# Kernel tuning notes

Hardware: AMD Instinct MI355X
Metric: run time of the kernel (lower is better)

## Reference

```python
import jax, jax.numpy as jnp
import numpy as np

D = 1024
H = 16
DK = D // H
HID = 4096
EPS = 1e-5


def setup_inputs() -> dict:
    key = jax.random.key(0)
    ks = jax.random.split(key, 16)
    B, S = 2, 2048
    sc = lambda fan_in: 1.0 / np.sqrt(fan_in)
    inp = {
        "x": jax.random.normal(ks[0], (B, S, D), jnp.float32),
        "y": jax.random.normal(ks[1], (B, S, D), jnp.float32),
        "mask": jnp.ones((B, 1, 1, S), jnp.int32),
        # attention projections, stored [in, out]
        "Wq": jax.random.normal(ks[2], (D, D), jnp.float32) * sc(D),
        "bq": jnp.zeros((D,), jnp.float32),
        "Wk": jax.random.normal(ks[3], (D, D), jnp.float32) * sc(D),
        "bk": jnp.zeros((D,), jnp.float32),
        "Wv": jax.random.normal(ks[4], (D, D), jnp.float32) * sc(D),
        "bv": jnp.zeros((D,), jnp.float32),
        "Wo": jax.random.normal(ks[5], (D, D), jnp.float32) * sc(D),
        "bo": jnp.zeros((D,), jnp.float32),
        # FFN
        "W1": jax.random.normal(ks[6], (D, HID), jnp.float32) * sc(D),
        "b1": jnp.zeros((HID,), jnp.float32),
        "W2": jax.random.normal(ks[7], (HID, D), jnp.float32) * sc(HID),
        "b2": jnp.zeros((D,), jnp.float32),
        # LayerNorms
        "g1": jnp.ones((D,), jnp.float32),
        "be1": jnp.zeros((D,), jnp.float32),
        "g2": jnp.ones((D,), jnp.float32),
        "be2": jnp.zeros((D,), jnp.float32),
    }
    return inp


def _layer_norm(x, g, b):
    m = jnp.mean(x, axis=-1, keepdims=True)
    v = jnp.mean(jnp.square(x - m), axis=-1, keepdims=True)
    return (x - m) * jax.lax.rsqrt(v + EPS) * g + b


def _split_heads(t):  # [B,S,D] -> [B,H,S,DK]
    B, S, _ = t.shape
    return t.reshape(B, S, H, DK).transpose(0, 2, 1, 3)


def reference(x, y, mask, Wq, bq, Wk, bk, Wv, bv, Wo, bo,
              W1, b1, W2, b2, g1, be1, g2, be2):
    scale = 1.0 / np.sqrt(DK)
    Q = _split_heads(x @ Wq + bq)
    K = _split_heads(y @ Wk + bk)
    V = _split_heads(y @ Wv + bv)
    scores = jnp.einsum("bhqd,bhkd->bhqk", Q, K) * scale  # [B,H,S,S]
    scores = jnp.where(mask == 0, jnp.float32(-1e9), scores)
    probs = jax.nn.softmax(scores, axis=-1)
    attn = jnp.einsum("bhqk,bhkd->bhqd", probs, V)
    B, _, S, _ = attn.shape
    attn = attn.transpose(0, 2, 1, 3).reshape(B, S, D)
    mha_out = attn @ Wo + bo
    x1 = _layer_norm(x + mha_out, g1, be1)
    ff = jax.nn.relu(x1 @ W1 + b1) @ W2 + b2
    return _layer_norm(x1 + ff, g2, be2)
```

## Files before the change

### kernel.cpp

```cpp
#include <hip/hip_runtime.h>

#define S_ 2048
#define D_ 1024
#define B_ 2
#define H_ 16
#define DK_ 64
#define HID_ 4096

typedef unsigned short u16;
typedef __attribute__((ext_vector_type(8))) short short8;
typedef __attribute__((ext_vector_type(4))) short s16x4;
typedef __attribute__((ext_vector_type(4))) float f32x4;

#define SLOT(q16, r16) (((q16) * 16) + ((r16) ^ (q16)))

__device__ __forceinline__ float bf2f(u16 u) {
  return __uint_as_float(((unsigned int)u) << 16);
}
__device__ __forceinline__ u16 f2bf(float f) {
  unsigned int x = __float_as_uint(f);
  x += 0x7fff + ((x >> 16) & 1);
  return (u16)(x >> 16);
}
__device__ __forceinline__ unsigned int pk2bf(float lo, float hi) {
  return ((__float_as_uint(lo) + 0x8000u) >> 16) | ((__float_as_uint(hi) + 0x8000u) & 0xffff0000u);
}

__device__ __forceinline__ f32x4 mfma16(s16x4 a, s16x4 b, f32x4 c) {
#if __has_builtin(__builtin_amdgcn_mfma_f32_16x16x16_bf16)
  return __builtin_amdgcn_mfma_f32_16x16x16_bf16(a, b, c, 0, 0, 0);
#else
  return __builtin_amdgcn_mfma_f32_16x16x16bf16_1k(a, b, c, 0, 0, 0);
#endif
}

__global__ void prep_k(
    const float* __restrict__ Wq, const float* __restrict__ Wk,
    const float* __restrict__ Wv, const float* __restrict__ Wo,
    const float* __restrict__ W1, const float* __restrict__ W2,
    u16* __restrict__ WqT, u16* __restrict__ WkT, u16* __restrict__ WvT,
    u16* __restrict__ WoT, u16* __restrict__ W1T, u16* __restrict__ W2T) {
  const int z = blockIdx.z;
  __shared__ u16 tile[32][33];
  const float* in; u16* outp; int R, C;
  switch (z) {
    case 0: in = Wq; outp = WqT; R = 1024; C = 1024; break;
    case 1: in = Wk; outp = WkT; R = 1024; C = 1024; break;
    case 2: in = Wv; outp = WvT; R = 1024; C = 1024; break;
    case 3: in = Wo; outp = WoT; R = 1024; C = 1024; break;
    case 4: in = W1; outp = W1T; R = 1024; C = 4096; break;
    default: in = W2; outp = W2T; R = 4096; C = 1024; break;
  }
  int c0, r0;
  if (z == 5) { c0 = blockIdx.y * 32; r0 = blockIdx.x * 32; }
  else        { c0 = blockIdx.x * 32; r0 = blockIdx.y * 32; }
  if (c0 >= C || r0 >= R) return;
  const int tx = threadIdx.x, ty = threadIdx.y;
  for (int i = ty; i < 32; i += 8)
    tile[i][tx] = f2bf(in[(long)(r0 + i) * C + c0 + tx]);
  __syncthreads();
  for (int i = ty; i < 32; i += 8)
    outp[(long)(c0 + i) * R + r0 + tx] = tile[tx][i];
}

__global__ __launch_bounds__(256) void cvt2_k(const float* __restrict__ x, const float* __restrict__ y,
                                              u16* __restrict__ xb, u16* __restrict__ yb) {
  const int z = blockIdx.y;
  const float* in = z ? y : x;
  u16* outp = z ? yb : xb;
  const int i = blockIdx.x * 256 + threadIdx.x;
  float4 v = ((const float4*)in)[i];
  unsigned int lo = (unsigned int)f2bf(v.x) | ((unsigned int)f2bf(v.y) << 16);
  unsigned int hi = (unsigned int)f2bf(v.z) | ((unsigned int)f2bf(v.w) << 16);
  ((uint2*)outp)[i] = make_uint2(lo, hi);
}

template<int MT, int NT, int OUTF32>
__global__ __launch_bounds__(256) void gemm_bt(
    const u16* __restrict__ A, const u16* __restrict__ Bt,
    const float* __restrict__ bias, void* __restrict__ Cv,
    int K, int lda, int ldb, int ldc,
    long sA, long sB, long sC, int relu) {
  constexpr int BM = MT * 32;
  constexpr int BN = NT * 32;
  __shared__ __align__(16) u16 As[BM * 32];
  __shared__ __align__(16) u16 Bs[BN * 32];
  const int z = blockIdx.z;
  A  += (long)z * sA;
  Bt += (long)z * sB;
  const int tid  = threadIdx.x;
  const int lane = tid & 63, wave = tid >> 6;
  const int quad = lane >> 4, l15 = lane & 15;
  const int wm = wave >> 1, wn = wave & 1;
  const u16* Ab = A  + (long)(blockIdx.y * BM) * lda;
  const u16* Bb = Bt + (long)(blockIdx.x * BN) * ldb;

  f32x4 acc[MT][NT];
#pragma unroll
  for (int i = 0; i < MT; ++i)
#pragma unroll
    for (int j = 0; j < NT; ++j) acc[i][j] = (f32x4){0.f, 0.f, 0.f, 0.f};

  const int r0  = tid >> 2;
  const int kk0 = (tid & 3) * 8;

  for (int kt = 0; kt < K; kt += 32) {
#pragma unroll
    for (int p = 0; p < BM / 64; ++p) {
      __builtin_amdgcn_global_load_lds(
          (const __attribute__((address_space(1))) void*)(Ab + (long)(p * 64 + r0) * lda + kt + kk0),
          (__attribute__((address_space(3))) void*)(&As[p * 2048 + tid * 8]), 16, 0, 0);
    }
#pragma unroll
    for (int p = 0; p < BN / 64; ++p) {
      __builtin_amdgcn_global_load_lds(
          (const __attribute__((address_space(1))) void*)(Bb + (long)(p * 64 + r0) * ldb + kt + kk0),
          (__attribute__((address_space(3))) void*)(&Bs[p * 2048 + tid * 8]), 16, 0, 0);
    }
    __syncthreads();
    short8 af[MT], bfr[NT];
#pragma unroll
    for (int mt = 0; mt < MT; ++mt)
      af[mt] = *(const short8*)&As[(wm * (MT * 16) + mt * 16 + l15) * 32 + quad * 8];
#pragma unroll
    for (int nt = 0; nt < NT; ++nt)
      bfr[nt] = *(const short8*)&Bs[(wn * (NT * 16) + nt * 16 + l15) * 32 + quad * 8];
#pragma unroll
    for (int mt = 0; mt < MT; ++mt)
#pragma unroll
      for (int nt = 0; nt < NT; ++nt)
        acc[mt][nt] = __builtin_amdgcn_mfma_f32_16x16x32_bf16(af[mt], bfr[nt], acc[mt][nt], 0, 0, 0);
    __syncthreads();
  }

#pragma unroll
  for (int nt = 0; nt < NT; ++nt) {
    const int col = blockIdx.x * BN + wn * (NT * 16) + nt * 16 + l15;
    const float bvv = bias ? bias[col] : 0.f;
#pragma unroll
    for (int mt = 0; mt < MT; ++mt) {
#pragma unroll
      for (int r = 0; r < 4; ++r) {
        const int row = blockIdx.y * BM + wm * (MT * 16) + mt * 16 + quad * 4 + r;
        float v = acc[mt][nt][r] + bvv;
        if (relu) v = fmaxf(v, 0.f);
        if (OUTF32) ((float*)Cv)[(long)z * sC + (long)row * ldc + col] = v;
        else        ((u16*)Cv)[(long)z * sC + (long)row * ldc + col] = f2bf(v);
      }
    }
  }
}

template<int RELU, int MODE>
__global__ __launch_bounds__(512, 2) void gemm256_k(
    const u16* __restrict__ A, const u16* __restrict__ Bt,
    const float* __restrict__ bias, u16* __restrict__ C,
    int K, int lda, int ldb, int ldc, int kOff, long sC) {
  __shared__ __align__(16) u16 lds[65536];
  int bx, by, z;
  if (MODE == 1) {
    const int gid = blockIdx.y * 16 + blockIdx.x;
    const int xcd = gid & 7, idx = gid >> 3;
    by = (xcd & 3) * 4 + (idx & 3);
    bx = (xcd >> 2) * 8 + (idx >> 2);
    z = 0;
  } else if (MODE == 2) {
    const int gid = (blockIdx.z * 16 + blockIdx.y) * 4 + blockIdx.x;
    const int xcd = gid & 7, idx = gid >> 3;
    z = idx >> 3;
    const int sub = idx & 7;
    by = xcd * 2 + (sub & 1);
    bx = sub >> 1;
  } else {
    bx = blockIdx.x; by = blockIdx.y; z = blockIdx.z;
  }
  A  += (long)z * kOff;
  Bt += (long)z * kOff;
  const int tid = threadIdx.x;
  const int lane = tid & 63, w = tid >> 6;
  const int quad = lane >> 4, l15 = lane & 15;
  const int wm = w >> 2, wn = w & 3;

  const int srow = w * 16 + l15;
  const u16* a0p = A + (long)(by * 256 + srow) * lda + quad * 8;
  const u16* a1p = a0p + (long)128 * lda;
  const u16* b0p = Bt + (long)(bx * 256 + srow) * ldb + quad * 8;
  const u16* b1p = b0p + (long)128 * ldb;

  f32x4 acc[8][4];
#pragma unroll
  for (int i = 0; i < 8; ++i)
#pragma unroll
    for (int j = 0; j < 4; ++j) acc[i][j] = (f32x4){0.f, 0.f, 0.f, 0.f};

  auto STAGE = [&](int c) {
    const int sl = (c & 3) * 8192;
    const long ko = (long)c * 32;
    __builtin_amdgcn_global_load_lds(
        (const __attribute__((address_space(1))) void*)(a0p + ko),
        (__attribute__((address_space(3))) void*)(&lds[sl + tid * 8]), 16, 0, 0);
    __builtin_amdgcn_global_load_lds(
        (const __attribute__((address_space(1))) void*)(a1p + ko),
        (__attribute__((address_space(3))) void*)(&lds[sl + 4096 + tid * 8]), 16, 0, 0);
    __builtin_amdgcn_global_load_lds(
        (const __attribute__((address_space(1))) void*)(b0p + ko),
        (__attribute__((address_space(3))) void*)(&lds[32768 + sl + tid * 8]), 16, 0, 0);
    __builtin_amdgcn_global_load_lds(
        (const __attribute__((address_space(1))) void*)(b1p + ko),
        (__attribute__((address_space(3))) void*)(&lds[32768 + sl + 4096 + tid * 8]), 16, 0, 0);
  };

  auto COMPUTE = [&](int t) {
    const int sl = (t & 3) * 8192;
    short8 af[8], bfv[4];
#pragma unroll
    for (int fr = 0; fr < 8; ++fr)
      af[fr] = *(const short8*)&lds[sl + ((wm * 8 + fr) * 64 + lane) * 8];
#pragma unroll
    for (int fc = 0; fc < 4; ++fc)
      bfv[fc] = *(const short8*)&lds[32768 + sl + ((wn * 4 + fc) * 64 + lane) * 8];
    __builtin_amdgcn_s_setprio(1);
#pragma unroll
    for (int fr = 0; fr < 8; ++fr)
#pragma unroll
      for (int fc = 0; fc < 4; ++fc)
        acc[fr][fc] = __builtin_amdgcn_mfma_f32_16x16x32_bf16(af[fr], bfv[fc], acc[fr][fc], 0, 0, 0);
    __builtin_amdgcn_s_setprio(0);
  };

  const int NT = K >> 5;
  STAGE(0); STAGE(1); STAGE(2);
  for (int t = 0; t < NT - 2; ++t) {
    asm volatile("s_waitcnt vmcnt(8)" ::: "memory");
    __builtin_amdgcn_s_barrier();
    __builtin_amdgcn_sched_barrier(0);
    if (t + 3 < NT) STAGE(t + 3);
    COMPUTE(t);
  }
  asm volatile("s_waitcnt vmcnt(4)" ::: "memory");
  __builtin_amdgcn_s_barrier();
  __builtin_amdgcn_sched_barrier(0);
  COMPUTE(NT - 2);
  asm volatile("s_waitcnt vmcnt(0)" ::: "memory");
  __builtin_amdgcn_s_barrier();
  __builtin_amdgcn_sched_barrier(0);
  COMPUTE(NT - 1);

  C += (long)z * sC;
#pragma unroll
  for (int fc = 0; fc < 4; ++fc) {
    const int col = bx * 256 + wn * 64 + fc * 16 + l15;
    const float bvv = bias ? bias[col] : 0.f;
#pragma unroll
    for (int fr = 0; fr < 8; ++fr) {
      const long row = by * 256 + wm * 128 + fr * 16 + quad * 4;
#pragma unroll
      for (int r = 0; r < 4; ++r) {
        float v = acc[fr][fc][r] + bvv;
        if (RELU) v = fmaxf(v, 0.f);
        C[(row + r) * ldc + col] = f2bf(v);
      }
    }
  }
}

__global__ __launch_bounds__(256) void qkv_k(
    const u16* __restrict__ xb, const u16* __restrict__ yb,
    const u16* __restrict__ WqT, const u16* __restrict__ WkT, const u16* __restrict__ WvT,
    const float* __restrict__ bq, const float* __restrict__ bk, const float* __restrict__ bv,
    u16* __restrict__ Q, u16* __restrict__ Kp, u16* __restrict__ Vp) {
  __shared__ __align__(16) u16 As[128 * 32];
  __shared__ __align__(16) u16 Bs[128 * 32];
  const int z = blockIdx.z;
  const u16* A  = (z == 0) ? xb : yb;
  const u16* Bt = (z == 0) ? WqT : (z == 1) ? WkT : WvT;
  const float* bias = (z == 0) ? bq : (z == 1) ? bk : bv;
  u16* C = (z == 0) ? Q : (z == 1) ? Kp : Vp;
  const float sc = (z == 0) ? 0.18033688011112042f : 1.0f;
  const int tid  = threadIdx.x;
  const int lane = tid & 63, wave = tid >> 6;
  const int quad = lane >> 4, l15 = lane & 15;
  const int wm = wave >> 1, wn = wave & 1;
  const u16* Ab = A  + (long)(blockIdx.y * 128) * D_;
  const u16* Bb = Bt + (long)(blockIdx.x * 128) * D_;

  f32x4 acc[4][4];
#pragma unroll
  for (int i = 0; i < 4; ++i)
#pragma unroll
    for (int j = 0; j < 4; ++j) acc[i][j] = (f32x4){0.f, 0.f, 0.f, 0.f};

  const int r0  = tid >> 2;
  const int kk0 = (tid & 3) * 8;

  for (int kt = 0; kt < D_; kt += 32) {
#pragma unroll
    for (int p = 0; p < 2; ++p) {
      __builtin_amdgcn_global_load_lds(
          (const __attribute__((address_space(1))) void*)(Ab + (long)(p * 64 + r0) * D_ + kt + kk0),
          (__attribute__((address_space(3))) void*)(&As[p * 2048 + tid * 8]), 16, 0, 0);
      __builtin_amdgcn_global_load_lds(
          (const __attribute__((address_space(1))) void*)(Bb + (long)(p * 64 + r0) * D_ + kt + kk0),
          (__attribute__((address_space(3))) void*)(&Bs[p * 2048 + tid * 8]), 16, 0, 0);
    }
    __syncthreads();
    short8 af[4], bfr[4];
#pragma unroll
    for (int mt = 0; mt < 4; ++mt)
      af[mt] = *(const short8*)&As[(wm * 64 + mt * 16 + l15) * 32 + quad * 8];
#pragma unroll
    for (int nt = 0; nt < 4; ++nt)
      bfr[nt] = *(const short8*)&Bs[(wn * 64 + nt * 16 + l15) * 32 + quad * 8];
#pragma unroll
    for (int mt = 0; mt < 4; ++mt)
#pragma unroll
      for (int nt = 0; nt < 4; ++nt)
        acc[mt][nt] = __builtin_amdgcn_mfma_f32_16x16x32_bf16(af[mt], bfr[nt], acc[mt][nt], 0, 0, 0);
    __syncthreads();
  }

#pragma unroll
  for (int nt = 0; nt < 4; ++nt) {
    const int col = blockIdx.x * 128 + wn * 64 + nt * 16 + l15;
    const float bvv = bias[col];
#pragma unroll
    for (int mt = 0; mt < 4; ++mt) {
#pragma unroll
      for (int r = 0; r < 4; ++r) {
        const int row = blockIdx.y * 128 + wm * 64 + mt * 16 + quad * 4 + r;
        C[(long)row * D_ + col] = f2bf((acc[mt][nt][r] + bvv) * sc);
      }
    }
  }
}

__global__ void vtrans_k(const u16* __restrict__ V, u16* __restrict__ Vt) {
  __shared__ u16 tile[32][33];
  const int bh = blockIdx.z, b = bh >> 4, h = bh & 15;
  const u16* in = V + (long)b * S_ * D_ + h * DK_;
  u16* outp = Vt + (long)bh * DK_ * S_;
  const int s0 = blockIdx.x * 32, d0 = blockIdx.y * 32;
  const int tx = threadIdx.x, ty = threadIdx.y;
  for (int i = ty; i < 32; i += 8)
    tile[i][tx] = in[(long)(s0 + i) * D_ + d0 + tx];
  __syncthreads();
  for (int i = ty; i < 32; i += 8)
    outp[(long)(d0 + i) * S_ + s0 + tx] = tile[tx][i];
}

__global__ __launch_bounds__(256, 4) void flash_k(
    const u16* __restrict__ Q, const u16* __restrict__ Kp, const u16* __restrict__ Vt,
    const int* __restrict__ mask, u16* __restrict__ ctx) {
  __shared__ __align__(16) u16 sQ[8192];
  __shared__ __align__(16) u16 sK[2][2048];
  __shared__ __align__(16) u16 sV[2][2048];
  __shared__ int s_allones;

  const int bh = blockIdx.x, qt = blockIdx.y;
  const int b = bh >> 4, h = bh & 15;
  const int tid = threadIdx.x;
  const int w = tid >> 6, lane = tid & 63;
  const int quad = lane >> 4, l15 = lane & 15;

  const u16* Qg  = Q  + ((long)b * S_ + qt * 128) * D_ + h * DK_;
  const u16* Kg  = Kp + (long)b * S_ * D_ + h * DK_;
  const u16* Vtg = Vt + (long)bh * DK_ * S_;
  const int* maskg = mask + (long)b * S_;
  u16* ctxg = ctx + ((long)b * S_ + qt * 128) * D_ + h * DK_;

  const int krow = tid >> 3, kc = tid & 7;
  const u16* kptr = Kg + (long)krow * D_ + kc * 8;
  const int ksw = (((krow >> 4) * 2 + (kc >> 2)) * 64 + SLOT(kc & 3, krow & 15)) * 8;
  const int vd  = ((tid >> 6) << 4) | (tid & 15);
  const int vq4 = ((tid >> 4) & 3) * 4;
  const u16* vptr = Vtg + (long)vd * S_ + vq4;

  uint4 kreg = *(const uint4*)kptr;
  uint2 vlo = *(const uint2*)vptr;
  uint2 vhi = *(const uint2*)(vptr + 16);

  int part = 1;
  for (int i = tid; i < S_; i += 256) part &= (maskg[i] != 0);
  if (tid == 0) s_allones = 1;

#pragma unroll
  for (int p = 0; p < 4; ++p) {
    const int idx = p * 256 + tid;
    const int row = idx >> 3, cb = idx & 7;
    uint4 v = *(const uint4*)(Qg + (long)row * D_ + cb * 8);
    *(uint4*)&sQ[(((row >> 4) * 2 + (cb >> 2)) * 64 + SLOT(cb & 3, row & 15)) * 8] = v;
  }
  *(uint4*)&sK[0][ksw] = kreg;
  *(uint4*)&sV[0][tid * 8] = make_uint4(vlo.x, vlo.y, vhi.x, vhi.y);
  kreg = *(const uint4*)(kptr + 32 * D_);
  vlo = *(const uint2*)(vptr + 32);
  vhi = *(const uint2*)(vptr + 48);
  kptr += 64 * D_;
  vptr += 64;
  __syncthreads();

  const int rslot = SLOT(quad, l15) * 8;

  short8 qf[2][2];
#pragma unroll
  for (int mf = 0; mf < 2; ++mf)
#pragma unroll
    for (int kt = 0; kt < 2; ++kt)
      qf[mf][kt] = *(const short8*)&sQ[(((w * 2 + mf) * 2 + kt) * 64) * 8 + rslot];

  if (!part) s_allones = 0;
  __syncthreads();
  const int allones = s_allones;

  float lsum[2] = {0.f, 0.f};
  f32x4 accOT[2][4];
#pragma unroll
  for (int i = 0; i < 2; ++i)
#pragma unroll
    for (int j = 0; j < 4; ++j) accOT[i][j] = (f32x4){0.f, 0.f, 0.f, 0.f};

  for (int t = 0; t < 64; ++t) {
    if (t) __syncthreads();
    const int buf = t & 1, nb = buf ^ 1;
    if (t < 63) {
      *(uint4*)&sK[nb][ksw] = kreg;
      *(uint4*)&sV[nb][tid * 8] = make_uint4(vlo.x, vlo.y, vhi.x, vhi.y);
      if (t < 62) {
        kreg = *(const uint4*)kptr;
        vlo = *(const uint2*)vptr;
        vhi = *(const uint2*)(vptr + 16);
        kptr += 32 * D_;
        vptr += 32;
      }
    }
    f32x4 accS[2][2];
#pragma unroll
    for (int i = 0; i < 2; ++i)
#pragma unroll
      for (int j = 0; j < 2; ++j) accS[i][j] = (f32x4){0.f, 0.f, 0.f, 0.f};
#pragma unroll
    for (int kt = 0; kt < 2; ++kt) {
      short8 kf0 = *(const short8*)&sK[buf][(kt * 64) * 8 + rslot];
      short8 kf1 = *(const short8*)&sK[buf][((2 + kt) * 64) * 8 + rslot];
#pragma unroll
      for (int mf = 0; mf < 2; ++mf) {
        accS[0][mf] = __builtin_amdgcn_mfma_f32_16x16x32_bf16(kf0, qf[mf][kt], accS[0][mf], 0, 0, 0);
        accS[1][mf] = __builtin_amdgcn_mfma_f32_16x16x32_bf16(kf1, qf[mf][kt], accS[1][mf], 0, 0, 0);
      }
    }
    s16x4 pb[2][2];
    if (allones) {
#pragma unroll
      for (int mk = 0; mk < 2; ++mk)
#pragma unroll
        for (int mf = 0; mf < 2; ++mf) {
          float p0 = __builtin_amdgcn_exp2f(accS[mk][mf][0]);
          float p1 = __builtin_amdgcn_exp2f(accS[mk][mf][1]);
          float p2 = __builtin_amdgcn_exp2f(accS[mk][mf][2]);
          float p3 = __builtin_amdgcn_exp2f(accS[mk][mf][3]);
          lsum[mf] += (p0 + p1) + (p2 + p3);
          *(uint2*)&pb[mk][mf] = make_uint2(pk2bf(p0, p1), pk2bf(p2, p3));
        }
    } else {
      const int4 mv0 = *(const int4*)(maskg + t * 32 + quad * 4);
      const int4 mv1 = *(const int4*)(maskg + t * 32 + 16 + quad * 4);
#pragma unroll
      for (int mk = 0; mk < 2; ++mk) {
        const int4 mv = mk ? mv1 : mv0;
#pragma unroll
        for (int mf = 0; mf < 2; ++mf) {
          float p0 = mv.x ? __builtin_amdgcn_exp2f(accS[mk][mf][0]) : 0.f;
          float p1 = mv.y ? __builtin_amdgcn_exp2f(accS[mk][mf][1]) : 0.f;
          float p2 = mv.z ? __builtin_amdgcn_exp2f(accS[mk][mf][2]) : 0.f;
          float p3 = mv.w ? __builtin_amdgcn_exp2f(accS[mk][mf][3]) : 0.f;
          lsum[mf] += (p0 + p1) + (p2 + p3);
          *(uint2*)&pb[mk][mf] = make_uint2(pk2bf(p0, p1), pk2bf(p2, p3));
        }
      }
    }
#pragma unroll
    for (int n = 0; n < 4; ++n) {
      short8 vv = *(const short8*)&sV[buf][(n * 64 + lane) * 8];
      s16x4 v0 = __builtin_shufflevector(vv, vv, 0, 1, 2, 3);
      s16x4 v1 = __builtin_shufflevector(vv, vv, 4, 5, 6, 7);
#pragma unroll
      for (int mf = 0; mf < 2; ++mf) {
        accOT[mf][n] = mfma16(v0, pb[0][mf], accOT[mf][n]);
        accOT[mf][n] = mfma16(v1, pb[1][mf], accOT[mf][n]);
      }
    }
  }

#pragma unroll
  for (int mf = 0; mf < 2; ++mf) {
    lsum[mf] += __shfl_xor(lsum[mf], 16, 64);
    lsum[mf] += __shfl_xor(lsum[mf], 32, 64);
  }
  const float inv0 = 1.f / lsum[0], inv1 = 1.f / lsum[1];
#pragma unroll
  for (int mf = 0; mf < 2; ++mf) {
    const float iv = mf ? inv1 : inv0;
    u16* cp = ctxg + (long)(w * 32 + mf * 16 + l15) * D_;
#pragma unroll
    for (int n = 0; n < 4; ++n) {
      float o0 = accOT[mf][n][0] * iv;
      float o1 = accOT[mf][n][1] * iv;
      float o2 = accOT[mf][n][2] * iv;
      float o3 = accOT[mf][n][3] * iv;
      *(uint2*)(cp + n * 16 + quad * 4) = make_uint2(pk2bf(o0, o1), pk2bf(o2, o3));
    }
  }
}

__device__ __forceinline__ float block_reduce_sum(float v, float* red) {
#pragma unroll
  for (int off = 32; off; off >>= 1) v += __shfl_down(v, off, 64);
  __syncthreads();
  if ((threadIdx.x & 63) == 0) red[threadIdx.x >> 6] = v;
  __syncthreads();
  return red[0] + red[1] + red[2] + red[3];
}

__global__ __launch_bounds__(256) void addln_fb(const float* __restrict__ A,
    const u16* __restrict__ M0, const u16* __restrict__ M1, const float* __restrict__ bo,
    const float* __restrict__ g, const float* __restrict__ be, u16* __restrict__ outp) {
  __shared__ float red[4];
  const int row = blockIdx.x, tid = threadIdx.x;
  const float4 av = ((const float4*)(A + (long)row * D_))[tid];
  const uint2 m0 = ((const uint2*)(M0 + (long)row * D_))[tid];
  const uint2 m1 = ((const uint2*)(M1 + (long)row * D_))[tid];
  const int c0 = tid * 4;
  float xv[4];
  xv[0] = av.x + bf2f((u16)(m0.x & 0xffff)) + bf2f((u16)(m1.x & 0xffff)) + bo[c0 + 0];
  xv[1] = av.y + bf2f((u16)(m0.x >> 16))    + bf2f((u16)(m1.x >> 16))    + bo[c0 + 1];
  xv[2] = av.z + bf2f((u16)(m0.y & 0xffff)) + bf2f((u16)(m1.y & 0xffff)) + bo[c0 + 2];
  xv[3] = av.w + bf2f((u16)(m0.y >> 16))    + bf2f((u16)(m1.y >> 16))    + bo[c0 + 3];
  float s  = xv[0] + xv[1] + xv[2] + xv[3];
  float ss = xv[0]*xv[0] + xv[1]*xv[1] + xv[2]*xv[2] + xv[3]*xv[3];
  s  = block_reduce_sum(s, red);
  ss = block_reduce_sum(ss, red);
  const float m   = s * (1.0f / 1024.0f);
  const float var = ss * (1.0f / 1024.0f) - m * m;
  const float rs  = rsqrtf(var + 1e-5f);
  float v0 = (xv[0] - m) * rs * g[c0 + 0] + be[c0 + 0];
  float v1 = (xv[1] - m) * rs * g[c0 + 1] + be[c0 + 1];
  float v2 = (xv[2] - m) * rs * g[c0 + 2] + be[c0 + 2];
  float v3 = (xv[3] - m) * rs * g[c0 + 3] + be[c0 + 3];
  unsigned int o01 = (unsigned int)f2bf(v0) | ((unsigned int)f2bf(v1) << 16);
  unsigned int o23 = (unsigned int)f2bf(v2) | ((unsigned int)f2bf(v3) << 16);
  ((uint2*)(outp + (long)row * D_))[tid] = make_uint2(o01, o23);
}

__global__ __launch_bounds__(256) void addln2_bf(const u16* __restrict__ A,
    const u16* __restrict__ F0, const u16* __restrict__ F1,
    const u16* __restrict__ F2, const u16* __restrict__ F3,
    const float* __restrict__ b2,
    const float* __restrict__ g, const float* __restrict__ be, float* __restrict__ outp) {
  __shared__ float red[4];
  const int row = blockIdx.x, tid = threadIdx.x;
  const uint2 av = ((const uint2*)(A + (long)row * D_))[tid];
  const uint2 f0 = ((const uint2*)(F0 + (long)row * D_))[tid];
  const uint2 f1 = ((const uint2*)(F1 + (long)row * D_))[tid];
  const uint2 f2 = ((const uint2*)(F2 + (long)row * D_))[tid];
  const uint2 f3 = ((const uint2*)(F3 + (long)row * D_))[tid];
  const int c0 = tid * 4;
  float xv[4];
  xv[0] = bf2f((u16)(av.x & 0xffff)) + bf2f((u16)(f0.x & 0xffff)) + bf2f((u16)(f1.x & 0xffff))
        + bf2f((u16)(f2.x & 0xffff)) + bf2f((u16)(f3.x & 0xffff)) + b2[c0 + 0];
  xv[1] = bf2f((u16)(av.x >> 16))    + bf2f((u16)(f0.x >> 16))    + bf2f((u16)(f1.x >> 16))
        + bf2f((u16)(f2.x >> 16))    + bf2f((u16)(f3.x >> 16))    + b2[c0 + 1];
  xv[2] = bf2f((u16)(av.y & 0xffff)) + bf2f((u16)(f0.y & 0xffff)) + bf2f((u16)(f1.y & 0xffff))
        + bf2f((u16)(f2.y & 0xffff)) + bf2f((u16)(f3.y & 0xffff)) + b2[c0 + 2];
  xv[3] = bf2f((u16)(av.y >> 16))    + bf2f((u16)(f0.y >> 16))    + bf2f((u16)(f1.y >> 16))
        + bf2f((u16)(f2.y >> 16))    + bf2f((u16)(f3.y >> 16))    + b2[c0 + 3];
  float s  = xv[0] + xv[1] + xv[2] + xv[3];
  float ss = xv[0]*xv[0] + xv[1]*xv[1] + xv[2]*xv[2] + xv[3]*xv[3];
  s  = block_reduce_sum(s, red);
  ss = block_reduce_sum(ss, red);
  const float m   = s * (1.0f / 1024.0f);
  const float var = ss * (1.0f / 1024.0f) - m * m;
  const float rs  = rsqrtf(var + 1e-5f);
  float4 o;
  o.x = (xv[0] - m) * rs * g[c0 + 0] + be[c0 + 0];
  o.y = (xv[1] - m) * rs * g[c0 + 1] + be[c0 + 1];
  o.z = (xv[2] - m) * rs * g[c0 + 2] + be[c0 + 2];
  o.w = (xv[3] - m) * rs * g[c0 + 3] + be[c0 + 3];
  ((float4*)(outp + (long)row * D_))[tid] = o;
}

extern "C" void kernel_launch(void* const* d_in, const int* in_sizes, int n_in,
                              void* d_out, int out_size, void* d_ws, size_t ws_size,
                              hipStream_t stream) {
  const float* x   = (const float*)d_in[0];
  const float* y   = (const float*)d_in[1];
  const int* mask  = (const int*)d_in[2];
  const float* Wq = (const float*)d_in[3];  const float* bq = (const float*)d_in[4];
  const float* Wk = (const float*)d_in[5];  const float* bk = (const float*)d_in[6];
  const float* Wv = (const float*)d_in[7];  const float* bv = (const float*)d_in[8];
  const float* Wo = (const float*)d_in[9];  const float* bo = (const float*)d_in[10];
  const float* W1 = (const float*)d_in[11]; const float* b1 = (const float*)d_in[12];
  const float* W2 = (const float*)d_in[13]; const float* b2 = (const float*)d_in[14];
  const float* g1 = (const float*)d_in[15]; const float* be1 = (const float*)d_in[16];
  const float* g2 = (const float*)d_in[17]; const float* be2 = (const float*)d_in[18];
  float* out = (float*)d_out;

  char* w = (char*)d_ws;
  const size_t MB = 1024 * 1024;
  u16* WqT = (u16*)(w + 0 * MB);
  u16* WkT = (u16*)(w + 2 * MB);
  u16* WvT = (u16*)(w + 4 * MB);
  u16* WoT = (u16*)(w + 6 * MB);
  u16* W1T = (u16*)(w + 8 * MB);
  u16* W2T = (u16*)(w + 16 * MB);
  u16* xb  = (u16*)(w + 24 * MB);
  u16* yb  = (u16*)(w + 32 * MB);
  u16* Q   = (u16*)(w + 40 * MB);
  u16* Kp  = (u16*)(w + 48 * MB);
  u16* Vp  = (u16*)(w + 56 * MB);
  u16* Vt  = (u16*)(w + 64 * MB);
  u16* ctx = (u16*)(w + 72 * MB);
  u16* mha = (u16*)(w + 80 * MB);
  u16* x1  = (u16*)(w + 24 * MB);
  u16* h1  = (u16*)(w + 96 * MB);
  u16* ff  = (u16*)(w + 40 * MB);

  prep_k<<<dim3(128, 32, 6), dim3(32, 8), 0, stream>>>(Wq, Wk, Wv, Wo, W1, W2,
      WqT, WkT, WvT, WoT, W1T, W2T);
  cvt2_k<<<dim3(4096, 2), 256, 0, stream>>>(x, y, xb, yb);

  qkv_k<<<dim3(8, 32, 3), 256, 0, stream>>>(xb, yb, WqT, WkT, WvT, bq, bk, bv, Q, Kp, Vp);

  vtrans_k<<<dim3(64, 2, 32), dim3(32, 8), 0, stream>>>(Vp, Vt);

  flash_k<<<dim3(32, 16), 256, 0, stream>>>(Q, Kp, Vt, mask, ctx);

  gemm_bt<4, 4, 0><<<dim3(8, 32, 2), 256, 0, stream>>>(ctx, WoT, nullptr, mha,
      512, 1024, 1024, 1024, 512, 512, (long)4096 * 1024, 0);
  addln_fb<<<dim3(4096), 256, 0, stream>>>(x, mha, mha + (long)4096 * 1024, bo, g1, be1, x1);

  gemm256_k<1, 1><<<dim3(16, 16, 1), 512, 0, stream>>>(x1, W1T, b1, h1,
      1024, 1024, 1024, 4096, 0, 0);
  gemm256_k<0, 2><<<dim3(4, 16, 4), 512, 0, stream>>>(h1, W2T, nullptr, ff,
      1024, 4096, 4096, 1024, 1024, (long)4096 * 1024);
  addln2_bf<<<dim3(4096), 256, 0, stream>>>(x1, ff, ff + (long)4096 * 1024,
      ff + (long)2 * 4096 * 1024, ff + (long)3 * 4096 * 1024, b2, g2, be2, out);
}
```

Measured before the change: 397.0 us.

## Halve flash attention query tile and drop XCD-aware GEMM block remapping

The flash attention kernel now handles 64 query rows per block instead of 128, so each wave covers 16 rows and the grid doubles to 1024 blocks. This cuts registers and shared memory per block and may allow higher occupancy. In exchange, K/V tiles are loaded twice as often per query row. Separately, the FFN GEMMs drop their XCD-aware block-index swizzle and use plain blockIdx mapping, which gives up L2 locality across chiplets.

```diff
diff --git a/kernel.cpp b/kernel.cpp
--- a/kernel.cpp
+++ b/kernel.cpp
@@ -151,29 +151,13 @@
   }
 }
 
-template<int RELU, int MODE>
+template<int RELU>
 __global__ __launch_bounds__(512, 2) void gemm256_k(
     const u16* __restrict__ A, const u16* __restrict__ Bt,
     const float* __restrict__ bias, u16* __restrict__ C,
     int K, int lda, int ldb, int ldc, int kOff, long sC) {
   __shared__ __align__(16) u16 lds[65536];
-  int bx, by, z;
-  if (MODE == 1) {
-    const int gid = blockIdx.y * 16 + blockIdx.x;
-    const int xcd = gid & 7, idx = gid >> 3;
-    by = (xcd & 3) * 4 + (idx & 3);
-    bx = (xcd >> 2) * 8 + (idx >> 2);
-    z = 0;
-  } else if (MODE == 2) {
-    const int gid = (blockIdx.z * 16 + blockIdx.y) * 4 + blockIdx.x;
-    const int xcd = gid & 7, idx = gid >> 3;
-    z = idx >> 3;
-    const int sub = idx & 7;
-    by = xcd * 2 + (sub & 1);
-    bx = sub >> 1;
-  } else {
-    bx = blockIdx.x; by = blockIdx.y; z = blockIdx.z;
-  }
+  const int bx = blockIdx.x, by = blockIdx.y, z = blockIdx.z;
   A  += (long)z * kOff;
   Bt += (long)z * kOff;
   const int tid = threadIdx.x;
@@ -351,7 +335,7 @@
 __global__ __launch_bounds__(256, 4) void flash_k(
     const u16* __restrict__ Q, const u16* __restrict__ Kp, const u16* __restrict__ Vt,
     const int* __restrict__ mask, u16* __restrict__ ctx) {
-  __shared__ __align__(16) u16 sQ[8192];
+  __shared__ __align__(16) u16 sQ[4096];
   __shared__ __align__(16) u16 sK[2][2048];
   __shared__ __align__(16) u16 sV[2][2048];
   __shared__ int s_allones;
@@ -362,11 +346,11 @@
   const int w = tid >> 6, lane = tid & 63;
   const int quad = lane >> 4, l15 = lane & 15;
 
-  const u16* Qg  = Q  + ((long)b * S_ + qt * 128) * D_ + h * DK_;
+  const u16* Qg  = Q  + ((long)b * S_ + qt * 64) * D_ + h * DK_;
   const u16* Kg  = Kp + (long)b * S_ * D_ + h * DK_;
   const u16* Vtg = Vt + (long)bh * DK_ * S_;
   const int* maskg = mask + (long)b * S_;
-  u16* ctxg = ctx + ((long)b * S_ + qt * 128) * D_ + h * DK_;
+  u16* ctxg = ctx + ((long)b * S_ + qt * 64) * D_ + h * DK_;
 
   const int krow = tid >> 3, kc = tid & 7;
   const u16* kptr = Kg + (long)krow * D_ + kc * 8;
@@ -384,7 +368,7 @@
   if (tid == 0) s_allones = 1;
 
 #pragma unroll
-  for (int p = 0; p < 4; ++p) {
+  for (int p = 0; p < 2; ++p) {
     const int idx = p * 256 + tid;
     const int row = idx >> 3, cb = idx & 7;
     uint4 v = *(const uint4*)(Qg + (long)row * D_ + cb * 8);
@@ -401,23 +385,19 @@
 
   const int rslot = SLOT(quad, l15) * 8;
 
-  short8 qf[2][2];
-#pragma unroll
-  for (int mf = 0; mf < 2; ++mf)
-#pragma unroll
-    for (int kt = 0; kt < 2; ++kt)
-      qf[mf][kt] = *(const short8*)&sQ[(((w * 2 + mf) * 2 + kt) * 64) * 8 + rslot];
+  short8 qf[2];
+#pragma unroll
+  for (int kt = 0; kt < 2; ++kt)
+    qf[kt] = *(const short8*)&sQ[((w * 2 + kt) * 64) * 8 + rslot];
 
   if (!part) s_allones = 0;
   __syncthreads();
   const int allones = s_allones;
 
-  float lsum[2] = {0.f, 0.f};
-  f32x4 accOT[2][4];
-#pragma unroll
-  for (int i = 0; i < 2; ++i)
-#pragma unroll
-    for (int j = 0; j < 4; ++j) accOT[i][j] = (f32x4){0.f, 0.f, 0.f, 0.f};
+  float lsum = 0.f;
+  f32x4 accOT[4];
+#pragma unroll
+  for (int j = 0; j < 4; ++j) accOT[j] = (f32x4){0.f, 0.f, 0.f, 0.f};
 
   for (int t = 0; t < 64; ++t) {
     if (t) __syncthreads();
@@ -433,49 +413,39 @@
         vptr += 32;
       }
     }
-    f32x4 accS[2][2];
-#pragma unroll
-    for (int i = 0; i < 2; ++i)
-#pragma unroll
-      for (int j = 0; j < 2; ++j) accS[i][j] = (f32x4){0.f, 0.f, 0.f, 0.f};
+    f32x4 accS[2];
+    accS[0] = (f32x4){0.f, 0.f, 0.f, 0.f};
+    accS[1] = (f32x4){0.f, 0.f, 0.f, 0.f};
 #pragma unroll
     for (int kt = 0; kt < 2; ++kt) {
       short8 kf0 = *(const short8*)&sK[buf][(kt * 64) * 8 + rslot];
       short8 kf1 = *(const short8*)&sK[buf][((2 + kt) * 64) * 8 + rslot];
-#pragma unroll
-      for (int mf = 0; mf < 2; ++mf) {
-        accS[0][mf] = __builtin_amdgcn_mfma_f32_16x16x32_bf16(kf0, qf[mf][kt], accS[0][mf], 0, 0, 0);
-        accS[1][mf] = __builtin_amdgcn_mfma_f32_16x16x32_bf16(kf1, qf[mf][kt], accS[1][mf], 0, 0, 0);
+      accS[0] = __builtin_amdgcn_mfma_f32_16x16x32_bf16(kf0, qf[kt], accS[0], 0, 0, 0);
+      accS[1] = __builtin_amdgcn_mfma_f32_16x16x32_bf16(kf1, qf[kt], accS[1], 0, 0, 0);
+    }
+    s16x4 pb[2];
+    if (allones) {
+#pragma unroll
+      for (int mk = 0; mk < 2; ++mk) {
+        float p0 = __builtin_amdgcn_exp2f(accS[mk][0]);
+        float p1 = __builtin_amdgcn_exp2f(accS[mk][1]);
+        float p2 = __builtin_amdgcn_exp2f(accS[mk][2]);
+        float p3 = __builtin_amdgcn_exp2f(accS[mk][3]);
+        lsum += (p0 + p1) + (p2 + p3);
+        *(uint2*)&pb[mk] = make_uint2(pk2bf(p0, p1), pk2bf(p2, p3));
       }
-    }
-    s16x4 pb[2][2];
-    if (allones) {
-#pragma unroll
-      for (int mk = 0; mk < 2; ++mk)
-#pragma unroll
-        for (int mf = 0; mf < 2; ++mf) {
-          float p0 = __builtin_amdgcn_exp2f(accS[mk][mf][0]);
-          float p1 = __builtin_amdgcn_exp2f(accS[mk][mf][1]);
-          float p2 = __builtin_amdgcn_exp2f(accS[mk][mf][2]);
-          float p3 = __builtin_amdgcn_exp2f(accS[mk][mf][3]);
-          lsum[mf] += (p0 + p1) + (p2 + p3);
-          *(uint2*)&pb[mk][mf] = make_uint2(pk2bf(p0, p1), pk2bf(p2, p3));
-        }
     } else {
       const int4 mv0 = *(const int4*)(maskg + t * 32 + quad * 4);
       const int4 mv1 = *(const int4*)(maskg + t * 32 + 16 + quad * 4);
 #pragma unroll
       for (int mk = 0; mk < 2; ++mk) {
         const int4 mv = mk ? mv1 : mv0;
-#pragma unroll
-        for (int mf = 0; mf < 2; ++mf) {
-          float p0 = mv.x ? __builtin_amdgcn_exp2f(accS[mk][mf][0]) : 0.f;
-          float p1 = mv.y ? __builtin_amdgcn_exp2f(accS[mk][mf][1]) : 0.f;
-          float p2 = mv.z ? __builtin_amdgcn_exp2f(accS[mk][mf][2]) : 0.f;
-          float p3 = mv.w ? __builtin_amdgcn_exp2f(accS[mk][mf][3]) : 0.f;
-          lsum[mf] += (p0 + p1) + (p2 + p3);
-          *(uint2*)&pb[mk][mf] = make_uint2(pk2bf(p0, p1), pk2bf(p2, p3));
-        }
+        float p0 = mv.x ? __builtin_amdgcn_exp2f(accS[mk][0]) : 0.f;
+        float p1 = mv.y ? __builtin_amdgcn_exp2f(accS[mk][1]) : 0.f;
+        float p2 = mv.z ? __builtin_amdgcn_exp2f(accS[mk][2]) : 0.f;
+        float p3 = mv.w ? __builtin_amdgcn_exp2f(accS[mk][3]) : 0.f;
+        lsum += (p0 + p1) + (p2 + p3);
+        *(uint2*)&pb[mk] = make_uint2(pk2bf(p0, p1), pk2bf(p2, p3));
       }
     }
 #pragma unroll
@@ -483,32 +453,22 @@
       short8 vv = *(const short8*)&sV[buf][(n * 64 + lane) * 8];
       s16x4 v0 = __builtin_shufflevector(vv, vv, 0, 1, 2, 3);
       s16x4 v1 = __builtin_shufflevector(vv, vv, 4, 5, 6, 7);
-#pragma unroll
-      for (int mf = 0; mf < 2; ++mf) {
-        accOT[mf][n] = mfma16(v0, pb[0][mf], accOT[mf][n]);
-        accOT[mf][n] = mfma16(v1, pb[1][mf], accOT[mf][n]);
-      }
-    }
-  }
-
-#pragma unroll
-  for (int mf = 0; mf < 2; ++mf) {
-    lsum[mf] += __shfl_xor(lsum[mf], 16, 64);
-    lsum[mf] += __shfl_xor(lsum[mf], 32, 64);
-  }
-  const float inv0 = 1.f / lsum[0], inv1 = 1.f / lsum[1];
-#pragma unroll
-  for (int mf = 0; mf < 2; ++mf) {
-    const float iv = mf ? inv1 : inv0;
-    u16* cp = ctxg + (long)(w * 32 + mf * 16 + l15) * D_;
-#pragma unroll
-    for (int n = 0; n < 4; ++n) {
-      float o0 = accOT[mf][n][0] * iv;
-      float o1 = accOT[mf][n][1] * iv;
-      float o2 = accOT[mf][n][2] * iv;
-      float o3 = accOT[mf][n][3] * iv;
-      *(uint2*)(cp + n * 16 + quad * 4) = make_uint2(pk2bf(o0, o1), pk2bf(o2, o3));
-    }
+      accOT[n] = mfma16(v0, pb[0], accOT[n]);
+      accOT[n] = mfma16(v1, pb[1], accOT[n]);
+    }
+  }
+
+  lsum += __shfl_xor(lsum, 16, 64);
+  lsum += __shfl_xor(lsum, 32, 64);
+  const float iv = 1.f / lsum;
+  u16* cp = ctxg + (long)(w * 16 + l15) * D_;
+#pragma unroll
+  for (int n = 0; n < 4; ++n) {
+    float o0 = accOT[n][0] * iv;
+    float o1 = accOT[n][1] * iv;
+    float o2 = accOT[n][2] * iv;
+    float o3 = accOT[n][3] * iv;
+    *(uint2*)(cp + n * 16 + quad * 4) = make_uint2(pk2bf(o0, o1), pk2bf(o2, o3));
   }
 }
 
@@ -632,15 +592,15 @@
 
   vtrans_k<<<dim3(64, 2, 32), dim3(32, 8), 0, stream>>>(Vp, Vt);
 
-  flash_k<<<dim3(32, 16), 256, 0, stream>>>(Q, Kp, Vt, mask, ctx);
+  flash_k<<<dim3(32, 32), 256, 0, stream>>>(Q, Kp, Vt, mask, ctx);
 
   gemm_bt<4, 4, 0><<<dim3(8, 32, 2), 256, 0, stream>>>(ctx, WoT, nullptr, mha,
       512, 1024, 1024, 1024, 512, 512, (long)4096 * 1024, 0);
   addln_fb<<<dim3(4096), 256, 0, stream>>>(x, mha, mha + (long)4096 * 1024, bo, g1, be1, x1);
 
-  gemm256_k<1, 1><<<dim3(16, 16, 1), 512, 0, stream>>>(x1, W1T, b1, h1,
+  gemm256_k<1><<<dim3(16, 16, 1), 512, 0, stream>>>(x1, W1T, b1, h1,
       1024, 1024, 1024, 4096, 0, 0);
-  gemm256_k<0, 2><<<dim3(4, 16, 4), 512, 0, stream>>>(h1, W2T, nullptr, ff,
+  gemm256_k<0><<<dim3(4, 16, 4), 512, 0, stream>>>(h1, W2T, nullptr, ff,
       1024, 4096, 4096, 1024, 1024, (long)4096 * 1024);
   addln2_bf<<<dim3(4096), 256, 0, stream>>>(x1, ff, ff + (long)4096 * 1024,
       ff + (long)2 * 4096 * 1024, ff + (long)3 * 4096 * 1024, b2, g2, be2, out);
```

New measurement: 415.5 us. +4.7%, slower.

## Widen flash blocks to 512 threads, split K/V loading, fuse prep kernels

Applied to the files above, without the earlier changes.

The flash attention kernel now runs 512-thread blocks that each cover 256 query rows. The first half of the threads stages K tiles and the second half stages V tiles, so each thread issues a single load per iteration, and the grid is halved. The activation bf16 conversion is folded into the weight-transpose kernel to save one launch. The XCD-aware block remapping in the FFN GEMMs is removed in favour of plain block indices, which may hurt L2 locality across chiplets. Fewer, larger flash blocks also lower occupancy flexibility and CU coverage.

```diff
diff --git a/kernel.cpp b/kernel.cpp
--- a/kernel.cpp
+++ b/kernel.cpp
@@ -34,14 +34,28 @@
 #endif
 }
 
-__global__ void prep_k(
+__global__ void prep8_k(
     const float* __restrict__ Wq, const float* __restrict__ Wk,
     const float* __restrict__ Wv, const float* __restrict__ Wo,
     const float* __restrict__ W1, const float* __restrict__ W2,
+    const float* __restrict__ x, const float* __restrict__ y,
     u16* __restrict__ WqT, u16* __restrict__ WkT, u16* __restrict__ WvT,
-    u16* __restrict__ WoT, u16* __restrict__ W1T, u16* __restrict__ W2T) {
+    u16* __restrict__ WoT, u16* __restrict__ W1T, u16* __restrict__ W2T,
+    u16* __restrict__ xb, u16* __restrict__ yb) {
+  __shared__ u16 tile[32][33];
   const int z = blockIdx.z;
-  __shared__ u16 tile[32][33];
+  const int tx = threadIdx.x, ty = threadIdx.y;
+  if (z >= 6) {
+    const float* in = (z == 7) ? y : x;
+    u16* outp = (z == 7) ? yb : xb;
+    const int tid = ty * 32 + tx;
+    const long i = ((long)blockIdx.y * 128 + blockIdx.x) * 256 + tid;
+    float4 v = ((const float4*)in)[i];
+    unsigned int lo = (unsigned int)f2bf(v.x) | ((unsigned int)f2bf(v.y) << 16);
+    unsigned int hi = (unsigned int)f2bf(v.z) | ((unsigned int)f2bf(v.w) << 16);
+    ((uint2*)outp)[i] = make_uint2(lo, hi);
+    return;
+  }
   const float* in; u16* outp; int R, C;
   switch (z) {
     case 0: in = Wq; outp = WqT; R = 1024; C = 1024; break;
@@ -55,24 +69,11 @@
   if (z == 5) { c0 = blockIdx.y * 32; r0 = blockIdx.x * 32; }
   else        { c0 = blockIdx.x * 32; r0 = blockIdx.y * 32; }
   if (c0 >= C || r0 >= R) return;
-  const int tx = threadIdx.x, ty = threadIdx.y;
   for (int i = ty; i < 32; i += 8)
     tile[i][tx] = f2bf(in[(long)(r0 + i) * C + c0 + tx]);
   __syncthreads();
   for (int i = ty; i < 32; i += 8)
     outp[(long)(c0 + i) * R + r0 + tx] = tile[tx][i];
-}
-
-__global__ __launch_bounds__(256) void cvt2_k(const float* __restrict__ x, const float* __restrict__ y,
-                                              u16* __restrict__ xb, u16* __restrict__ yb) {
-  const int z = blockIdx.y;
-  const float* in = z ? y : x;
-  u16* outp = z ? yb : xb;
-  const int i = blockIdx.x * 256 + threadIdx.x;
-  float4 v = ((const float4*)in)[i];
-  unsigned int lo = (unsigned int)f2bf(v.x) | ((unsigned int)f2bf(v.y) << 16);
-  unsigned int hi = (unsigned int)f2bf(v.z) | ((unsigned int)f2bf(v.w) << 16);
-  ((uint2*)outp)[i] = make_uint2(lo, hi);
 }
 
 template<int MT, int NT, int OUTF32>
@@ -151,29 +152,13 @@
   }
 }
 
-template<int RELU, int MODE>
+template<int RELU>
 __global__ __launch_bounds__(512, 2) void gemm256_k(
     const u16* __restrict__ A, const u16* __restrict__ Bt,
     const float* __restrict__ bias, u16* __restrict__ C,
     int K, int lda, int ldb, int ldc, int kOff, long sC) {
   __shared__ __align__(16) u16 lds[65536];
-  int bx, by, z;
-  if (MODE == 1) {
-    const int gid = blockIdx.y * 16 + blockIdx.x;
-    const int xcd = gid & 7, idx = gid >> 3;
-    by = (xcd & 3) * 4 + (idx & 3);
-    bx = (xcd >> 2) * 8 + (idx >> 2);
-    z = 0;
-  } else if (MODE == 2) {
-    const int gid = (blockIdx.z * 16 + blockIdx.y) * 4 + blockIdx.x;
-    const int xcd = gid & 7, idx = gid >> 3;
-    z = idx >> 3;
-    const int sub = idx & 7;
-    by = xcd * 2 + (sub & 1);
-    bx = sub >> 1;
-  } else {
-    bx = blockIdx.x; by = blockIdx.y; z = blockIdx.z;
-  }
+  const int bx = blockIdx.x, by = blockIdx.y, z = blockIdx.z;
   A  += (long)z * kOff;
   Bt += (long)z * kOff;
   const int tid = threadIdx.x;
@@ -348,10 +333,10 @@
     outp[(long)(d0 + i) * S_ + s0 + tx] = tile[tx][i];
 }
 
-__global__ __launch_bounds__(256, 4) void flash_k(
+__global__ __launch_bounds__(512, 2) void flash_k(
     const u16* __restrict__ Q, const u16* __restrict__ Kp, const u16* __restrict__ Vt,
     const int* __restrict__ mask, u16* __restrict__ ctx) {
-  __shared__ __align__(16) u16 sQ[8192];
+  __shared__ __align__(16) u16 sQ[16384];
   __shared__ __align__(16) u16 sK[2][2048];
   __shared__ __align__(16) u16 sV[2][2048];
   __shared__ int s_allones;
@@ -362,41 +347,52 @@
   const int w = tid >> 6, lane = tid & 63;
   const int quad = lane >> 4, l15 = lane & 15;
 
-  const u16* Qg  = Q  + ((long)b * S_ + qt * 128) * D_ + h * DK_;
+  const u16* Qg  = Q  + ((long)b * S_ + qt * 256) * D_ + h * DK_;
   const u16* Kg  = Kp + (long)b * S_ * D_ + h * DK_;
   const u16* Vtg = Vt + (long)bh * DK_ * S_;
   const int* maskg = mask + (long)b * S_;
-  u16* ctxg = ctx + ((long)b * S_ + qt * 128) * D_ + h * DK_;
-
-  const int krow = tid >> 3, kc = tid & 7;
-  const u16* kptr = Kg + (long)krow * D_ + kc * 8;
+  u16* ctxg = ctx + ((long)b * S_ + qt * 256) * D_ + h * DK_;
+
+  const int isK = tid < 256;
+  const int t2 = tid & 255;
+  const int krow = t2 >> 3, kc = t2 & 7;
+  const int vd  = ((t2 >> 6) << 4) | (t2 & 15);
+  const int vq4 = ((t2 >> 4) & 3) * 4;
+  const u16* gptr = isK ? (Kg + (long)krow * D_ + kc * 8)
+                        : (Vtg + (long)vd * S_ + vq4);
+  const long gstep = isK ? (long)32 * D_ : (long)32;
   const int ksw = (((krow >> 4) * 2 + (kc >> 2)) * 64 + SLOT(kc & 3, krow & 15)) * 8;
-  const int vd  = ((tid >> 6) << 4) | (tid & 15);
-  const int vq4 = ((tid >> 4) & 3) * 4;
-  const u16* vptr = Vtg + (long)vd * S_ + vq4;
-
-  uint4 kreg = *(const uint4*)kptr;
-  uint2 vlo = *(const uint2*)vptr;
-  uint2 vhi = *(const uint2*)(vptr + 16);
+  u16* sdst0 = isK ? &sK[0][ksw] : &sV[0][t2 * 8];
+  u16* sdst1 = isK ? &sK[1][ksw] : &sV[1][t2 * 8];
+
+  auto gload = [&](const u16* p) {
+    uint4 r;
+    if (isK) {
+      r = *(const uint4*)p;
+    } else {
+      uint2 lo = *(const uint2*)p;
+      uint2 hi = *(const uint2*)(p + 16);
+      r = make_uint4(lo.x, lo.y, hi.x, hi.y);
+    }
+    return r;
+  };
+
+  uint4 reg = gload(gptr);
 
   int part = 1;
-  for (int i = tid; i < S_; i += 256) part &= (maskg[i] != 0);
+  for (int i = tid; i < S_; i += 512) part &= (maskg[i] != 0);
   if (tid == 0) s_allones = 1;
 
 #pragma unroll
   for (int p = 0; p < 4; ++p) {
-    const int idx = p * 256 + tid;
+    const int idx = p * 512 + tid;
     const int row = idx >> 3, cb = idx & 7;
     uint4 v = *(const uint4*)(Qg + (long)row * D_ + cb * 8);
     *(uint4*)&sQ[(((row >> 4) * 2 + (cb >> 2)) * 64 + SLOT(cb & 3, row & 15)) * 8] = v;
   }
-  *(uint4*)&sK[0][ksw] = kreg;
-  *(uint4*)&sV[0][tid * 8] = make_uint4(vlo.x, vlo.y, vhi.x, vhi.y);
-  kreg = *(const uint4*)(kptr + 32 * D_);
-  vlo = *(const uint2*)(vptr + 32);
-  vhi = *(const uint2*)(vptr + 48);
-  kptr += 64 * D_;
-  vptr += 64;
+  *(uint4*)sdst0 = reg;
+  reg = gload(gptr + gstep);
+  gptr += 2 * gstep;
   __syncthreads();
 
   const int rslot = SLOT(quad, l15) * 8;
@@ -421,16 +417,12 @@
 
   for (int t = 0; t < 64; ++t) {
     if (t) __syncthreads();
-    const int buf = t & 1, nb = buf ^ 1;
+    const int buf = t & 1;
     if (t < 63) {
-      *(uint4*)&sK[nb][ksw] = kreg;
-      *(uint4*)&sV[nb][tid * 8] = make_uint4(vlo.x, vlo.y, vhi.x, vhi.y);
+      *(uint4*)((t & 1) ? sdst0 : sdst1) = reg;
       if (t < 62) {
-        kreg = *(const uint4*)kptr;
-        vlo = *(const uint2*)vptr;
-        vhi = *(const uint2*)(vptr + 16);
-        kptr += 32 * D_;
-        vptr += 32;
+        reg = gload(gptr);
+        gptr += gstep;
       }
     }
     f32x4 accS[2][2];
@@ -624,23 +616,22 @@
   u16* h1  = (u16*)(w + 96 * MB);
   u16* ff  = (u16*)(w + 40 * MB);
 
-  prep_k<<<dim3(128, 32, 6), dim3(32, 8), 0, stream>>>(Wq, Wk, Wv, Wo, W1, W2,
-      WqT, WkT, WvT, WoT, W1T, W2T);
-  cvt2_k<<<dim3(4096, 2), 256, 0, stream>>>(x, y, xb, yb);
+  prep8_k<<<dim3(128, 32, 8), dim3(32, 8), 0, stream>>>(Wq, Wk, Wv, Wo, W1, W2,
+      x, y, WqT, WkT, WvT, WoT, W1T, W2T, xb, yb);
 
   qkv_k<<<dim3(8, 32, 3), 256, 0, stream>>>(xb, yb, WqT, WkT, WvT, bq, bk, bv, Q, Kp, Vp);
 
   vtrans_k<<<dim3(64, 2, 32), dim3(32, 8), 0, stream>>>(Vp, Vt);
 
-  flash_k<<<dim3(32, 16), 256, 0, stream>>>(Q, Kp, Vt, mask, ctx);
+  flash_k<<<dim3(32, 8), 512, 0, stream>>>(Q, Kp, Vt, mask, ctx);
 
   gemm_bt<4, 4, 0><<<dim3(8, 32, 2), 256, 0, stream>>>(ctx, WoT, nullptr, mha,
       512, 1024, 1024, 1024, 512, 512, (long)4096 * 1024, 0);
   addln_fb<<<dim3(4096), 256, 0, stream>>>(x, mha, mha + (long)4096 * 1024, bo, g1, be1, x1);
 
-  gemm256_k<1, 1><<<dim3(16, 16, 1), 512, 0, stream>>>(x1, W1T, b1, h1,
+  gemm256_k<1><<<dim3(16, 16, 1), 512, 0, stream>>>(x1, W1T, b1, h1,
       1024, 1024, 1024, 4096, 0, 0);
-  gemm256_k<0, 2><<<dim3(4, 16, 4), 512, 0, stream>>>(h1, W2T, nullptr, ff,
+  gemm256_k<0><<<dim3(4, 16, 4), 512, 0, stream>>>(h1, W2T, nullptr, ff,
       1024, 4096, 4096, 1024, 1024, (long)4096 * 1024);
   addln2_bf<<<dim3(4096), 256, 0, stream>>>(x1, ff, ff + (long)4096 * 1024,
       ff + (long)2 * 4096 * 1024, ff + (long)3 * 4096 * 1024, b2, g2, be2, out);
```

Result: no change. 390.2 us (-1.7%).
